# Optimization experiments

Measured on AMD Instinct MI355X. Metric: run time of the kernel, lower is better.

Reference implementation:

```python
import jax, jax.numpy as jnp
import numpy as np

B, N, M = 4, 4096, 4096


def setup_inputs() -> dict:
    key = jax.random.key(0)
    k1, k2 = jax.random.split(key)
    source = jax.random.normal(k1, (B, N, 3), dtype=jnp.float32)
    target = jax.random.normal(k2, (B, M, 3), dtype=jnp.float32)
    return {"source": source, "target": target}


def reference(source, target):
    # Pairwise squared distances: dist[b, n, m] = ||source[b,n] - target[b,m]||^2
    x2 = jnp.sum(source * source, axis=-1)          # (B, N)
    y2 = jnp.sum(target * target, axis=-1)          # (B, M)
    xy = jnp.einsum('bnd,bmd->bnm', source, target)  # (B, N, M)
    dist = x2[:, :, None] + y2[:, None, :] - 2.0 * xy
    # bidirectional Chamfer (default args: bidirectional=True, reverse=False)
    loss_s2t = jnp.mean(jnp.min(dist, axis=2), axis=1)  # (B,)
    loss_t2s = jnp.mean(jnp.min(dist, axis=1), axis=1)  # (B,)
    return jnp.mean(loss_s2t + loss_t2s)
```

## Files before the change

kernel.cpp:

```cpp
#include <hip/hip_runtime.h>

typedef float f2 __attribute__((ext_vector_type(2)));

namespace {
constexpr int kB = 4;
constexpr int kN = 4096;
constexpr int kPts = kB * kN;
constexpr int kP = 2 * kPts;
constexpr int kBlk = 256;
constexpr int kSplit = 16;
constexpr int kChunk = kN / kSplit;
constexpr int kOP = 2;
constexpr float kInf = 3.4e38f;
}


__device__ __forceinline__ unsigned enc(float f) {
  unsigned u = __float_as_uint(f);
  return (u & 0x80000000u) ? ~u : (u | 0x80000000u);
}
__device__ __forceinline__ float dec(unsigned k) {
  return __uint_as_float((k & 0x80000000u) ? (k ^ 0x80000000u) : ~k);
}

__global__ __launch_bounds__(kBlk) void cham_prep_kernel(
    const float* __restrict__ src, const float* __restrict__ tgt,
    float4* __restrict__ pack4, unsigned* __restrict__ keys,
    float* __restrict__ out) {
  int g = blockIdx.x * kBlk + threadIdx.x;
  const float* p = (g < kPts / 2) ? (tgt + (size_t)g * 6)
                                  : (src + (size_t)(g - kPts / 2) * 6);
  const f2 a = *(const f2*)(p);
  const f2 bv = *(const f2*)(p + 2);
  const f2 c = *(const f2*)(p + 4);
  const float x0 = a.x, y0 = a.y, z0 = bv.x;
  const float x1 = bv.y, y1 = c.x, z1 = c.y;
  const float w0 = fmaf(x0, x0, fmaf(y0, y0, z0 * z0));
  const float w1 = fmaf(x1, x1, fmaf(y1, y1, z1 * z1));
  pack4[2 * g] = make_float4(x0, x1, y0, y1);
  pack4[2 * g + 1] = make_float4(z0, z1, w0, w1);
  ((uint2*)keys)[g] = make_uint2(0xFFFFFFFFu, 0xFFFFFFFFu);
  if (g == 0) out[0] = 0.0f;
}

__global__ __launch_bounds__(kBlk) void cham_min_kernel(
    const float4* __restrict__ pack4, unsigned* __restrict__ keys) {
  const int dir = blockIdx.z;
  const int b = blockIdx.y;
  const int chunk = blockIdx.x & (kSplit - 1);
  const int ntile = blockIdx.x >> 4;
  const int tp = ntile * kBlk + threadIdx.x;

  const size_t ownPair =
      ((size_t)(1 - dir) * kPts + (size_t)b * kN) / 2 + (size_t)tp;
  const float4 OA = pack4[2 * ownPair];
  const float4 OB = pack4[2 * ownPair + 1];
  const f2 NX0 = {-2.0f * OA.x, -2.0f * OA.x};
  const f2 NY0 = {-2.0f * OA.z, -2.0f * OA.z};
  const f2 NZ0 = {-2.0f * OB.x, -2.0f * OB.x};
  const f2 NX1 = {-2.0f * OA.y, -2.0f * OA.y};
  const f2 NY1 = {-2.0f * OA.w, -2.0f * OA.w};
  const f2 NZ1 = {-2.0f * OB.y, -2.0f * OB.y};

  const size_t g0 =
      ((size_t)dir * kPts + (size_t)b * kN + (size_t)chunk * kChunk) / 2;
  const float4* __restrict__ q = pack4 + 2 * g0;

  float e0a = kInf, e0b = kInf, e1a = kInf, e1b = kInf;
#pragma unroll 8
  for (int g = 0; g < kChunk / 2; ++g) {
    const float4 A = q[2 * g + 0];
    const float4 Bv = q[2 * g + 1];
    const f2 X = {A.x, A.y}, Y = {A.z, A.w}, Z = {Bv.x, Bv.y};
    f2 Wv = {Bv.z, Bv.w};
    f2 d0 = __builtin_elementwise_fma(
        NX0, X,
        __builtin_elementwise_fma(NY0, Y,
                                  __builtin_elementwise_fma(NZ0, Z, Wv)));
    f2 d1 = __builtin_elementwise_fma(
        NX1, X,
        __builtin_elementwise_fma(NY1, Y,
                                  __builtin_elementwise_fma(NZ1, Z, Wv)));
    if (g & 1) {
      e0b = fminf(fminf(d0.x, d0.y), e0b);
      e1b = fminf(fminf(d1.x, d1.y), e1b);
    } else {
      e0a = fminf(fminf(d0.x, d0.y), e0a);
      e1a = fminf(fminf(d1.x, d1.y), e1a);
    }
  }

  const float best0 = fminf(e0a, e0b) + OB.z;
  const float best1 = fminf(e1a, e1b) + OB.w;
  const unsigned kbase = ((unsigned)(dir * kB + b)) * kN + 2u * (unsigned)tp;
  atomicMin(&keys[kbase + 0], enc(best0));
  atomicMin(&keys[kbase + 1], enc(best1));
}

__global__ __launch_bounds__(kBlk) void cham_reduce_kernel(
    const unsigned* __restrict__ keys, float* __restrict__ out) {
  __shared__ float red[kBlk];
  float acc = 0.0f;
  for (int i = blockIdx.x * kBlk + threadIdx.x; i < kP; i += gridDim.x * kBlk)
    acc += dec(keys[i]);
  red[threadIdx.x] = acc;
  __syncthreads();
  for (int s = kBlk / 2; s > 0; s >>= 1) {
    if (threadIdx.x < s) red[threadIdx.x] += red[threadIdx.x + s];
    __syncthreads();
  }
  if (threadIdx.x == 0) atomicAdd(out, red[0] * (1.0f / kPts));
}

extern "C" void kernel_launch(void* const* d_in, const int* in_sizes, int n_in,
                              void* d_out, int out_size, void* d_ws,
                              size_t ws_size, hipStream_t stream) {
  const float* src = (const float*)d_in[0];
  const float* tgt = (const float*)d_in[1];
  float* out = (float*)d_out;

  unsigned* keys = (unsigned*)d_ws;
  float* packf = (float*)((char*)d_ws + (size_t)kP * 4);

  cham_prep_kernel<<<dim3(kP / 2 / kBlk), kBlk, 0, stream>>>(
      src, tgt, (float4*)packf, keys, out);

  dim3 grid(kN / (kBlk * kOP) * kSplit, kB, 2);
  cham_min_kernel<<<grid, kBlk, 0, stream>>>((const float4*)packf, keys);

  cham_reduce_kernel<<<dim3(16), kBlk, 0, stream>>>(keys, out);
}
```

Before: 71.54 us.

## Keep other-points in registers and broadcast own points with wave min-reduction

Each lane now holds 32 other-cloud points in registers, and each wave loops over 16 own points that are loaded uniformly across the wave. Every lane computes partial distances to its register set, then a 64-lane shuffle reduction finds the minimum per own point. This moves the reuse axis so the streamed other-point loads of the old kernel go away, and it cuts the number of atomicMin operations per key. The cost is extra shuffle-reduction work per own point and higher register pressure, with launch bounds set to allow three blocks per unit.

```diff
diff --git a/kernel.cpp b/kernel.cpp
--- a/kernel.cpp
+++ b/kernel.cpp
@@ -8,9 +8,11 @@
 constexpr int kPts = kB * kN;
 constexpr int kP = 2 * kPts;
 constexpr int kBlk = 256;
-constexpr int kSplit = 16;
-constexpr int kChunk = kN / kSplit;
-constexpr int kOP = 2;
+constexpr int kPairs = 16;
+constexpr int kOthersPerWave = 64 * 2 * kPairs;
+constexpr int kOSeg = kN / kOthersPerWave;
+constexpr int kOwnsPerWave = 16;
+constexpr int kOwnsPerBlk = 4 * kOwnsPerWave;
 constexpr float kInf = 3.4e38f;
 }
 
@@ -43,58 +45,72 @@
   if (g == 0) out[0] = 0.0f;
 }
 
-__global__ __launch_bounds__(kBlk) void cham_min_kernel(
+__global__ __launch_bounds__(kBlk, 3) void cham_min_kernel(
     const float4* __restrict__ pack4, unsigned* __restrict__ keys) {
   const int dir = blockIdx.z;
   const int b = blockIdx.y;
-  const int chunk = blockIdx.x & (kSplit - 1);
-  const int ntile = blockIdx.x >> 4;
-  const int tp = ntile * kBlk + threadIdx.x;
+  const int oseg = blockIdx.x & (kOSeg - 1);
+  const int ownBlk = blockIdx.x >> 1;
+  const int wave = threadIdx.x >> 6;
+  const int lane = threadIdx.x & 63;
 
-  const size_t ownPair =
-      ((size_t)(1 - dir) * kPts + (size_t)b * kN) / 2 + (size_t)tp;
-  const float4 OA = pack4[2 * ownPair];
-  const float4 OB = pack4[2 * ownPair + 1];
-  const f2 NX0 = {-2.0f * OA.x, -2.0f * OA.x};
-  const f2 NY0 = {-2.0f * OA.z, -2.0f * OA.z};
-  const f2 NZ0 = {-2.0f * OB.x, -2.0f * OB.x};
-  const f2 NX1 = {-2.0f * OA.y, -2.0f * OA.y};
-  const f2 NY1 = {-2.0f * OA.w, -2.0f * OA.w};
-  const f2 NZ1 = {-2.0f * OB.y, -2.0f * OB.y};
+  const size_t gBase = ((size_t)dir * kPts + (size_t)b * kN) / 2 +
+                       (size_t)oseg * (kOthersPerWave / 2);
+  f2 X2[kPairs], Y2[kPairs], Z2[kPairs], W2[kPairs];
+#pragma unroll
+  for (int r = 0; r < kPairs; ++r) {
+    const size_t gp = gBase + (size_t)(r * 64 + lane);
+    const float4 A = pack4[2 * gp];
+    const float4 Bv = pack4[2 * gp + 1];
+    X2[r] = f2{-2.0f * A.x, -2.0f * A.y};
+    Y2[r] = f2{-2.0f * A.z, -2.0f * A.w};
+    Z2[r] = f2{-2.0f * Bv.x, -2.0f * Bv.y};
+    W2[r] = f2{Bv.z, Bv.w};
+  }
 
-  const size_t g0 =
-      ((size_t)dir * kPts + (size_t)b * kN + (size_t)chunk * kChunk) / 2;
-  const float4* __restrict__ q = pack4 + 2 * g0;
+  const int own0 = ownBlk * kOwnsPerBlk + wave * kOwnsPerWave;
+  const size_t ownPt = (size_t)(1 - dir) * kPts + (size_t)b * kN + own0;
+  const float4* __restrict__ ownp = pack4 + ownPt;
+  unsigned* __restrict__ kb = keys + ((size_t)dir * kB + b) * kN + own0;
 
-  float e0a = kInf, e0b = kInf, e1a = kInf, e1b = kInf;
-#pragma unroll 8
-  for (int g = 0; g < kChunk / 2; ++g) {
-    const float4 A = q[2 * g + 0];
-    const float4 Bv = q[2 * g + 1];
-    const f2 X = {A.x, A.y}, Y = {A.z, A.w}, Z = {Bv.x, Bv.y};
-    f2 Wv = {Bv.z, Bv.w};
-    f2 d0 = __builtin_elementwise_fma(
-        NX0, X,
-        __builtin_elementwise_fma(NY0, Y,
-                                  __builtin_elementwise_fma(NZ0, Z, Wv)));
-    f2 d1 = __builtin_elementwise_fma(
-        NX1, X,
-        __builtin_elementwise_fma(NY1, Y,
-                                  __builtin_elementwise_fma(NZ1, Z, Wv)));
-    if (g & 1) {
-      e0b = fminf(fminf(d0.x, d0.y), e0b);
-      e1b = fminf(fminf(d1.x, d1.y), e1b);
-    } else {
-      e0a = fminf(fminf(d0.x, d0.y), e0a);
-      e1a = fminf(fminf(d1.x, d1.y), e1a);
+  for (int ob = 0; ob < kOwnsPerWave / 4; ++ob) {
+    float red[4], wo[4];
+#pragma unroll
+    for (int u = 0; u < 4; ++u) {
+      const int k = ob * 4 + u;
+      const float4 A = ownp[2 * (k >> 1)];
+      const float4 Bo = ownp[2 * (k >> 1) + 1];
+      const float x = (k & 1) ? A.y : A.x;
+      const float y = (k & 1) ? A.w : A.z;
+      const float z = (k & 1) ? Bo.y : Bo.x;
+      wo[u] = (k & 1) ? Bo.w : Bo.z;
+      const f2 dx = f2{x, x};
+      const f2 dy = f2{y, y};
+      const f2 dz = f2{z, z};
+      float ea = kInf, eb = kInf;
+#pragma unroll
+      for (int r = 0; r < kPairs; ++r) {
+        const f2 e = __builtin_elementwise_fma(
+            X2[r], dx,
+            __builtin_elementwise_fma(Y2[r], dy,
+                                      __builtin_elementwise_fma(Z2[r], dz,
+                                                                W2[r])));
+        if (r & 1) eb = fminf(fminf(e.x, e.y), eb);
+        else       ea = fminf(fminf(e.x, e.y), ea);
+      }
+      red[u] = fminf(ea, eb);
+    }
+#pragma unroll
+    for (int u = 0; u < 4; ++u)
+#pragma unroll
+      for (int m = 1; m < 64; m <<= 1)
+        red[u] = fminf(red[u], __shfl_xor(red[u], m, 64));
+    if (lane == 0) {
+#pragma unroll
+      for (int u = 0; u < 4; ++u)
+        atomicMin(&kb[ob * 4 + u], enc(red[u] + wo[u]));
     }
   }
-
-  const float best0 = fminf(e0a, e0b) + OB.z;
-  const float best1 = fminf(e1a, e1b) + OB.w;
-  const unsigned kbase = ((unsigned)(dir * kB + b)) * kN + 2u * (unsigned)tp;
-  atomicMin(&keys[kbase + 0], enc(best0));
-  atomicMin(&keys[kbase + 1], enc(best1));
 }
 
 __global__ __launch_bounds__(kBlk) void cham_reduce_kernel(
@@ -125,7 +141,7 @@
   cham_prep_kernel<<<dim3(kP / 2 / kBlk), kBlk, 0, stream>>>(
       src, tgt, (float4*)packf, keys, out);
 
-  dim3 grid(kN / (kBlk * kOP) * kSplit, kB, 2);
+  dim3 grid(kOSeg * (kN / kOwnsPerBlk), kB, 2);
   cham_min_kernel<<<grid, kBlk, 0, stream>>>((const float4*)packf, keys);
 
   cham_reduce_kernel<<<dim3(16), kBlk, 0, stream>>>(keys, out);
```

Result: slower. 83.55 us (+16.8%).

## Register-block four own points per thread and double the target split

Applied to the files above, without the earlier changes.

Each thread now keeps four own points in registers instead of two, so every loaded target pair is reused across twice as many distance evaluations. The target range is split into 32 chunks instead of 16, which keeps the grid at the same block count. The aim is to halve the global/L2 load traffic per FMA in the inner loop. The cost is more registers per thread and twice as many atomicMin operations per key, since each key now receives one update per chunk.

```diff
diff --git a/kernel.cpp b/kernel.cpp
--- a/kernel.cpp
+++ b/kernel.cpp
@@ -8,9 +8,9 @@
 constexpr int kPts = kB * kN;
 constexpr int kP = 2 * kPts;
 constexpr int kBlk = 256;
-constexpr int kSplit = 16;
+constexpr int kOP = 4;
+constexpr int kSplit = 32;
 constexpr int kChunk = kN / kSplit;
-constexpr int kOP = 2;
 constexpr float kInf = 3.4e38f;
 }
 
@@ -48,53 +48,59 @@
   const int dir = blockIdx.z;
   const int b = blockIdx.y;
   const int chunk = blockIdx.x & (kSplit - 1);
-  const int ntile = blockIdx.x >> 4;
-  const int tp = ntile * kBlk + threadIdx.x;
+  const int ntile = blockIdx.x >> 5;
+  const int n0 = (ntile * kBlk + threadIdx.x) * kOP;
 
   const size_t ownPair =
-      ((size_t)(1 - dir) * kPts + (size_t)b * kN) / 2 + (size_t)tp;
-  const float4 OA = pack4[2 * ownPair];
-  const float4 OB = pack4[2 * ownPair + 1];
-  const f2 NX0 = {-2.0f * OA.x, -2.0f * OA.x};
-  const f2 NY0 = {-2.0f * OA.z, -2.0f * OA.z};
-  const f2 NZ0 = {-2.0f * OB.x, -2.0f * OB.x};
-  const f2 NX1 = {-2.0f * OA.y, -2.0f * OA.y};
-  const f2 NY1 = {-2.0f * OA.w, -2.0f * OA.w};
-  const f2 NZ1 = {-2.0f * OB.y, -2.0f * OB.y};
+      ((size_t)(1 - dir) * kPts + (size_t)b * kN + n0) / 2;
+  const float4 A0 = pack4[2 * ownPair + 0];
+  const float4 B0 = pack4[2 * ownPair + 1];
+  const float4 A1 = pack4[2 * ownPair + 2];
+  const float4 B1 = pack4[2 * ownPair + 3];
+
+  const f2 NX[kOP] = {{-2.0f * A0.x, -2.0f * A0.x},
+                      {-2.0f * A0.y, -2.0f * A0.y},
+                      {-2.0f * A1.x, -2.0f * A1.x},
+                      {-2.0f * A1.y, -2.0f * A1.y}};
+  const f2 NY[kOP] = {{-2.0f * A0.z, -2.0f * A0.z},
+                      {-2.0f * A0.w, -2.0f * A0.w},
+                      {-2.0f * A1.z, -2.0f * A1.z},
+                      {-2.0f * A1.w, -2.0f * A1.w}};
+  const f2 NZ[kOP] = {{-2.0f * B0.x, -2.0f * B0.x},
+                      {-2.0f * B0.y, -2.0f * B0.y},
+                      {-2.0f * B1.x, -2.0f * B1.x},
+                      {-2.0f * B1.y, -2.0f * B1.y}};
+  const float wo[kOP] = {B0.z, B0.w, B1.z, B1.w};
 
   const size_t g0 =
       ((size_t)dir * kPts + (size_t)b * kN + (size_t)chunk * kChunk) / 2;
   const float4* __restrict__ q = pack4 + 2 * g0;
 
-  float e0a = kInf, e0b = kInf, e1a = kInf, e1b = kInf;
+  float ea[kOP], eb[kOP];
+#pragma unroll
+  for (int k = 0; k < kOP; ++k) { ea[k] = kInf; eb[k] = kInf; }
+
 #pragma unroll 8
   for (int g = 0; g < kChunk / 2; ++g) {
     const float4 A = q[2 * g + 0];
     const float4 Bv = q[2 * g + 1];
     const f2 X = {A.x, A.y}, Y = {A.z, A.w}, Z = {Bv.x, Bv.y};
-    f2 Wv = {Bv.z, Bv.w};
-    f2 d0 = __builtin_elementwise_fma(
-        NX0, X,
-        __builtin_elementwise_fma(NY0, Y,
-                                  __builtin_elementwise_fma(NZ0, Z, Wv)));
-    f2 d1 = __builtin_elementwise_fma(
-        NX1, X,
-        __builtin_elementwise_fma(NY1, Y,
-                                  __builtin_elementwise_fma(NZ1, Z, Wv)));
-    if (g & 1) {
-      e0b = fminf(fminf(d0.x, d0.y), e0b);
-      e1b = fminf(fminf(d1.x, d1.y), e1b);
-    } else {
-      e0a = fminf(fminf(d0.x, d0.y), e0a);
-      e1a = fminf(fminf(d1.x, d1.y), e1a);
+    const f2 Wv = {Bv.z, Bv.w};
+#pragma unroll
+    for (int k = 0; k < kOP; ++k) {
+      const f2 e = __builtin_elementwise_fma(
+          NX[k], X,
+          __builtin_elementwise_fma(NY[k], Y,
+                                    __builtin_elementwise_fma(NZ[k], Z, Wv)));
+      if (g & 1) eb[k] = fminf(fminf(e.x, e.y), eb[k]);
+      else       ea[k] = fminf(fminf(e.x, e.y), ea[k]);
     }
   }
 
-  const float best0 = fminf(e0a, e0b) + OB.z;
-  const float best1 = fminf(e1a, e1b) + OB.w;
-  const unsigned kbase = ((unsigned)(dir * kB + b)) * kN + 2u * (unsigned)tp;
-  atomicMin(&keys[kbase + 0], enc(best0));
-  atomicMin(&keys[kbase + 1], enc(best1));
+  unsigned* __restrict__ kb = keys + ((size_t)dir * kB + b) * kN + n0;
+#pragma unroll
+  for (int k = 0; k < kOP; ++k)
+    atomicMin(&kb[k], enc(fminf(ea[k], eb[k]) + wo[k]));
 }
 
 __global__ __launch_bounds__(kBlk) void cham_reduce_kernel(
```

Result: slower. 76.43 us (+6.8%).

## Replace atomicMin key reduction with per-split partial minima buffer

Applied to the files above, without the earlier changes.

Instead of encoding floats as sortable unsigned keys and doing atomicMin across the 16 target chunks, each chunk block writes its per-point minima to a dedicated partials slab. The reduce kernel then takes the min over the 16 splits for each point before summing. This removes atomic contention and the key-initialisation pass, but adds a 16x larger intermediate buffer that the small reduce grid must read.

```diff
diff --git a/kernel.cpp b/kernel.cpp
--- a/kernel.cpp
+++ b/kernel.cpp
@@ -8,25 +8,16 @@
 constexpr int kPts = kB * kN;
 constexpr int kP = 2 * kPts;
 constexpr int kBlk = 256;
+constexpr int kOP = 2;
 constexpr int kSplit = 16;
 constexpr int kChunk = kN / kSplit;
-constexpr int kOP = 2;
 constexpr float kInf = 3.4e38f;
 }
 
 
-__device__ __forceinline__ unsigned enc(float f) {
-  unsigned u = __float_as_uint(f);
-  return (u & 0x80000000u) ? ~u : (u | 0x80000000u);
-}
-__device__ __forceinline__ float dec(unsigned k) {
-  return __uint_as_float((k & 0x80000000u) ? (k ^ 0x80000000u) : ~k);
-}
-
 __global__ __launch_bounds__(kBlk) void cham_prep_kernel(
     const float* __restrict__ src, const float* __restrict__ tgt,
-    float4* __restrict__ pack4, unsigned* __restrict__ keys,
-    float* __restrict__ out) {
+    float4* __restrict__ pack4, float* __restrict__ out) {
   int g = blockIdx.x * kBlk + threadIdx.x;
   const float* p = (g < kPts / 2) ? (tgt + (size_t)g * 6)
                                   : (src + (size_t)(g - kPts / 2) * 6);
@@ -39,12 +30,11 @@
   const float w1 = fmaf(x1, x1, fmaf(y1, y1, z1 * z1));
   pack4[2 * g] = make_float4(x0, x1, y0, y1);
   pack4[2 * g + 1] = make_float4(z0, z1, w0, w1);
-  ((uint2*)keys)[g] = make_uint2(0xFFFFFFFFu, 0xFFFFFFFFu);
   if (g == 0) out[0] = 0.0f;
 }
 
 __global__ __launch_bounds__(kBlk) void cham_min_kernel(
-    const float4* __restrict__ pack4, unsigned* __restrict__ keys) {
+    const float4* __restrict__ pack4, float* __restrict__ partials) {
   const int dir = blockIdx.z;
   const int b = blockIdx.y;
   const int chunk = blockIdx.x & (kSplit - 1);
@@ -72,12 +62,12 @@
     const float4 A = q[2 * g + 0];
     const float4 Bv = q[2 * g + 1];
     const f2 X = {A.x, A.y}, Y = {A.z, A.w}, Z = {Bv.x, Bv.y};
-    f2 Wv = {Bv.z, Bv.w};
-    f2 d0 = __builtin_elementwise_fma(
+    const f2 Wv = {Bv.z, Bv.w};
+    const f2 d0 = __builtin_elementwise_fma(
         NX0, X,
         __builtin_elementwise_fma(NY0, Y,
                                   __builtin_elementwise_fma(NZ0, Z, Wv)));
-    f2 d1 = __builtin_elementwise_fma(
+    const f2 d1 = __builtin_elementwise_fma(
         NX1, X,
         __builtin_elementwise_fma(NY1, Y,
                                   __builtin_elementwise_fma(NZ1, Z, Wv)));
@@ -92,17 +82,24 @@
 
   const float best0 = fminf(e0a, e0b) + OB.z;
   const float best1 = fminf(e1a, e1b) + OB.w;
-  const unsigned kbase = ((unsigned)(dir * kB + b)) * kN + 2u * (unsigned)tp;
-  atomicMin(&keys[kbase + 0], enc(best0));
-  atomicMin(&keys[kbase + 1], enc(best1));
+  float2* __restrict__ pb =
+      (float2*)(partials + ((size_t)(dir * kB + b) * kSplit + chunk) * kN);
+  pb[tp] = make_float2(best0, best1);
 }
 
 __global__ __launch_bounds__(kBlk) void cham_reduce_kernel(
-    const unsigned* __restrict__ keys, float* __restrict__ out) {
+    const float* __restrict__ partials, float* __restrict__ out) {
   __shared__ float red[kBlk];
   float acc = 0.0f;
-  for (int i = blockIdx.x * kBlk + threadIdx.x; i < kP; i += gridDim.x * kBlk)
-    acc += dec(keys[i]);
+  for (int i = blockIdx.x * kBlk + threadIdx.x; i < kP; i += gridDim.x * kBlk) {
+    const int db = i >> 12;
+    const int n = i & (kN - 1);
+    const float* p = partials + ((size_t)db * kSplit) * kN + n;
+    float m = kInf;
+#pragma unroll
+    for (int s = 0; s < kSplit; ++s) m = fminf(m, p[(size_t)s * kN]);
+    acc += m;
+  }
   red[threadIdx.x] = acc;
   __syncthreads();
   for (int s = kBlk / 2; s > 0; s >>= 1) {
@@ -119,14 +116,15 @@
   const float* tgt = (const float*)d_in[1];
   float* out = (float*)d_out;
 
-  unsigned* keys = (unsigned*)d_ws;
-  float* packf = (float*)((char*)d_ws + (size_t)kP * 4);
+  float* partials = (float*)d_ws;
+  float* packf =
+      (float*)((char*)d_ws + (size_t)kP * kSplit * 4);
 
   cham_prep_kernel<<<dim3(kP / 2 / kBlk), kBlk, 0, stream>>>(
-      src, tgt, (float4*)packf, keys, out);
+      src, tgt, (float4*)packf, out);
 
   dim3 grid(kN / (kBlk * kOP) * kSplit, kB, 2);
-  cham_min_kernel<<<grid, kBlk, 0, stream>>>((const float4*)packf, keys);
+  cham_min_kernel<<<grid, kBlk, 0, stream>>>((const float4*)packf, partials);
 
-  cham_reduce_kernel<<<dim3(16), kBlk, 0, stream>>>(keys, out);
+  cham_reduce_kernel<<<dim3(16), kBlk, 0, stream>>>(partials, out);
 }
```

New measurement: 79.30 us. +10.9%, slower.
